# Performance work log

Measured on AMD Instinct MI355X. Metric: run time of the kernel, lower is better.

Reference implementation:

```python
import jax, jax.numpy as jnp
import numpy as np

B, C_IN, C_OUT, N, MODES = 16, 128, 128, 16384, 128

def setup_inputs() -> dict:
    key = jax.random.key(0)
    k1, k2, k3, k4 = jax.random.split(key, 4)
    scale = 1.0 / (C_IN * C_OUT)
    x = jax.random.normal(k1, (B, C_IN, N), dtype=jnp.float32)
    wbases = jax.random.normal(k2, (N, MODES), dtype=jnp.float32)
    bases = jax.random.normal(k3, (N, MODES), dtype=jnp.float32)
    W = scale * jax.random.uniform(k4, (C_IN, C_OUT, MODES), dtype=jnp.float32)
    return {"x": x, "wbases": wbases, "bases": bases, "W": W}

def reference(x, wbases, bases, W):
    # project onto weighted bases: [B, C_in, N] x [N, K] -> [B, C_in, K]
    x_co = jnp.einsum('bcx,xk->bck', x, wbases)
    # per-mode channel mixing: [B, C_in, K] x [C_in, C_out, K] -> [B, C_out, K]
    x_hat = jnp.einsum('bik,iok->bok', x_co, W)
    # reconstruct: [B, C_out, K] x [N, K] -> [B, C_out, N]
    return jnp.einsum('bok,xk->box', x_hat, bases)
```

## Files before the change

kernel.cpp:

```cpp
#include <hip/hip_runtime.h>
#include <hip/hip_bf16.h>
#include <stdint.h>

#define NB 16
#define NC 128
#define NK 128
#define NSP 16384
#define SPLIT 32
#define CHUNK 512

typedef float f32x4 __attribute__((ext_vector_type(4)));
typedef __bf16 bf16x8 __attribute__((ext_vector_type(8)));

__device__ __forceinline__ unsigned short f32_to_bf16(float a) {
  unsigned int u = __float_as_uint(a);
  return (unsigned short)((u + 0x7fffu + ((u >> 16) & 1u)) >> 16);
}

__device__ __forceinline__ unsigned int pack_bf16(float a, float b) {
  unsigned int ua = __float_as_uint(a);
  unsigned int ub = __float_as_uint(b);
  ua = (ua + 0x7fffu + ((ua >> 16) & 1u)) >> 16;
  ub = (ub + 0x7fffu + ((ub >> 16) & 1u)) & 0xffff0000u;
  return ua | ub;
}

__device__ __forceinline__ bf16x8 pack8(float4 a0, float4 a1) {
  uint4 u;
  u.x = pack_bf16(a0.x, a0.y);
  u.y = pack_bf16(a0.z, a0.w);
  u.z = pack_bf16(a1.x, a1.y);
  u.w = pack_bf16(a1.z, a1.w);
  return __builtin_bit_cast(bf16x8, u);
}

__device__ __forceinline__ void gl_lds16(const void* g, void* l) {
  __builtin_amdgcn_global_load_lds(
      (const __attribute__((address_space(1))) unsigned int*)g,
      (__attribute__((address_space(3))) unsigned int*)l, 16, 0, 0);
}

__global__ void k0_prep(const float* __restrict__ wb, unsigned short* __restrict__ wbT,
                        const float* __restrict__ bases, unsigned short* __restrict__ bb) {
  __shared__ float tile[32][33];
  if (blockIdx.x < 2048) {
    int bid = blockIdx.x;
    int kt = (bid & 3) * 32;
    int nt = (bid >> 2) * 32;
    int tx = threadIdx.x & 31;
    int ty = threadIdx.x >> 5;
#pragma unroll
    for (int i = 0; i < 32; i += 8)
      tile[ty + i][tx] = wb[(size_t)(nt + ty + i) * NK + kt + tx];
    __syncthreads();
#pragma unroll
    for (int i = 0; i < 32; i += 8)
      wbT[(size_t)(kt + ty + i) * NSP + nt + tx] = f32_to_bf16(tile[tx][ty + i]);
  } else {
    int i = (blockIdx.x - 2048) * 256 + threadIdx.x;
    float4 v = ((const float4*)bases)[i];
    uint2 o;
    o.x = pack_bf16(v.x, v.y);
    o.y = pack_bf16(v.z, v.w);
    ((uint2*)bb)[i] = o;
  }
}

__global__ __launch_bounds__(256, 4)
void k1_proj(const float* __restrict__ x, const unsigned short* __restrict__ wbT,
             float* __restrict__ part) {
  int blk = blockIdx.x;
  int chunk = blk & 31;
  int bc = blk >> 5;
  int b = bc >> 1;
  int chalf = bc & 1;
  int n0 = chunk * CHUNK;
  __shared__ __align__(16) char lds[2][16384];
  int tid = threadIdx.x;
  int lane = tid & 63;
  int wave = tid >> 6;
  int cbw = (wave & 1) * 32;
  int kbw = (wave >> 1) * 64;
  int r = lane & 15;
  int q = lane >> 4;

  f32x4 acc[2][4];
#pragma unroll
  for (int t = 0; t < 2; ++t)
#pragma unroll
    for (int u = 0; u < 4; ++u) acc[t][u] = (f32x4){0.f, 0.f, 0.f, 0.f};

  const float* aptr = x + (size_t)(b * NC + chalf * 64 + (lane >> 3)) * NSP +
                      n0 + ((lane & 7) ^ (lane >> 3)) * 4;
  const unsigned short* bptr =
      wbT + (size_t)(lane >> 2) * NSP + n0 + (lane & 3) * 8;

#pragma unroll
  for (int j = 0; j < 2; ++j) {
    int i = wave * 2 + j;
    gl_lds16(aptr + (size_t)(8 * i) * NSP, lds[0] + i * 1024);
    gl_lds16(bptr + (size_t)(16 * i) * NSP, lds[0] + 8192 + i * 1024);
  }
  __syncthreads();

#pragma unroll 2
  for (int it = 0; it < CHUNK / 32; ++it) {
    int cur = it & 1;
    if (it + 1 < CHUNK / 32) {
#pragma unroll
      for (int j = 0; j < 2; ++j) {
        int i = wave * 2 + j;
        gl_lds16(aptr + (size_t)(8 * i) * NSP + (it + 1) * 32,
                 lds[cur ^ 1] + i * 1024);
        gl_lds16(bptr + (size_t)(16 * i) * NSP + (it + 1) * 32,
                 lds[cur ^ 1] + 8192 + i * 1024);
      }
    }
    const char* La = lds[cur];
    const char* Lb = lds[cur] + 8192;
    bf16x8 af[2], bf[4];
#pragma unroll
    for (int t = 0; t < 2; ++t) {
      int rw = cbw + 16 * t + r;
      float4 f0 = *(const float4*)(La + rw * 128 + (((2 * q + 0) ^ (r & 7)) << 4));
      float4 f1 = *(const float4*)(La + rw * 128 + (((2 * q + 1) ^ (r & 7)) << 4));
      af[t] = pack8(f0, f1);
    }
#pragma unroll
    for (int u = 0; u < 4; ++u) {
      int rk = kbw + 16 * u + r;
      bf[u] = *(const bf16x8*)(Lb + rk * 64 + q * 16);
    }
#pragma unroll
    for (int t = 0; t < 2; ++t)
#pragma unroll
      for (int u = 0; u < 4; ++u)
        acc[t][u] = __builtin_amdgcn_mfma_f32_16x16x32_bf16(af[t], bf[u],
                                                            acc[t][u], 0, 0, 0);
    __syncthreads();
  }

  float* pp = part + (size_t)(b * SPLIT + chunk) * (NC * NK);
  int rq = q * 4;
#pragma unroll
  for (int t = 0; t < 2; ++t)
#pragma unroll
    for (int u = 0; u < 4; ++u)
#pragma unroll
      for (int v = 0; v < 4; ++v)
        pp[(chalf * 64 + cbw + 16 * t + rq + v) * NK + kbw + 16 * u + r] =
            acc[t][u][v];
}

__global__ __launch_bounds__(256)
void k1b_reduce(const float* __restrict__ part, float* __restrict__ x_co) {
  int idx = blockIdx.x * 256 + threadIdx.x;
  int b = idx >> 13;
  int r2 = idx & 8191;
  const float2* p = (const float2*)(part + (size_t)b * SPLIT * (NC * NK)) + r2;
  float2 s = {0.f, 0.f};
#pragma unroll
  for (int c = 0; c < SPLIT; ++c) {
    float2 v = p[(size_t)c * (NC * NK / 2)];
    s.x += v.x;
    s.y += v.y;
  }
  ((float2*)x_co)[idx] = s;
}

__global__ __launch_bounds__(128)
void k2_mix(const float* __restrict__ x_co, const float* __restrict__ W,
            unsigned short* __restrict__ xhat_bf) {
  int b = blockIdx.x >> 6;
  int o0 = (blockIdx.x & 63) * 2;
  int k = threadIdx.x;
  const float* xc = x_co + (size_t)b * NC * NK + k;
  const float* w0 = W + (size_t)o0 * NK + k;
  float a0 = 0.f, a1 = 0.f;
#pragma unroll 4
  for (int i = 0; i < NC; ++i) {
    float v = xc[(size_t)i * NK];
    a0 += v * w0[(size_t)i * (NC * NK)];
    a1 += v * w0[(size_t)i * (NC * NK) + NK];
  }
  size_t base = ((size_t)b * NC + o0) * NK + k;
  xhat_bf[base] = f32_to_bf16(a0);
  xhat_bf[base + NK] = f32_to_bf16(a1);
}

__global__ __launch_bounds__(256, 4)
void k3_recon(const unsigned short* __restrict__ xhat_bf,
              const unsigned short* __restrict__ bases_bf,
              float* __restrict__ out) {
  int blk = blockIdx.x;
  int mo0 = (blk & 15) * 128;
  int n0 = (blk >> 4) * 256;
  int tid = threadIdx.x;
  int lane = tid & 63;
  int wave = tid >> 6;
  int mb = (wave & 1) * 64;
  int nb = (wave >> 1) * 64;
  int r = lane & 15;
  int q = lane >> 4;
  int rq = q * 4;

  const unsigned short* arow = xhat_bf + (size_t)(mo0 + mb + r) * NK + q * 8;

#pragma unroll
  for (int sub = 0; sub < 2; ++sub) {
    const unsigned short* brow =
        bases_bf + (size_t)(n0 + sub * 128 + nb + r) * NK + q * 8;
    f32x4 acc[4][4];
#pragma unroll
    for (int t = 0; t < 4; ++t)
#pragma unroll
      for (int u = 0; u < 4; ++u) acc[t][u] = (f32x4){0.f, 0.f, 0.f, 0.f};
#pragma unroll
    for (int s = 0; s < 4; ++s) {
      bf16x8 af[4], bf[4];
#pragma unroll
      for (int t = 0; t < 4; ++t)
        af[t] = *(const bf16x8*)(arow + (size_t)t * 16 * NK + s * 32);
#pragma unroll
      for (int u = 0; u < 4; ++u)
        bf[u] = *(const bf16x8*)(brow + (size_t)u * 16 * NK + s * 32);
#pragma unroll
      for (int t = 0; t < 4; ++t)
#pragma unroll
        for (int u = 0; u < 4; ++u)
          acc[t][u] = __builtin_amdgcn_mfma_f32_16x16x32_bf16(af[t], bf[u],
                                                              acc[t][u], 0, 0, 0);
    }
    float* obase = out + (size_t)(mo0 + mb + rq) * NSP + n0 + sub * 128 + nb + r;
#pragma unroll
    for (int t = 0; t < 4; ++t)
#pragma unroll
      for (int u = 0; u < 4; ++u)
#pragma unroll
        for (int v = 0; v < 4; ++v)
          obase[(size_t)(16 * t + v) * NSP + 16 * u] = acc[t][u][v];
  }
}

extern "C" void kernel_launch(void* const* d_in, const int* in_sizes, int n_in,
                              void* d_out, int out_size, void* d_ws, size_t ws_size,
                              hipStream_t stream) {
  const float* x = (const float*)d_in[0];
  const float* wbases = (const float*)d_in[1];
  const float* bases = (const float*)d_in[2];
  const float* W = (const float*)d_in[3];
  float* out = (float*)d_out;

  char* ws = (char*)d_ws;
  if (ws_size < ((size_t)42 << 20)) return;
  unsigned short* wbT = (unsigned short*)(ws);
  unsigned short* bases_bf = (unsigned short*)(ws + ((size_t)4 << 20));
  float* part = (float*)(ws + ((size_t)8 << 20));
  float* x_co = (float*)(ws + ((size_t)40 << 20));
  unsigned short* xhat_bf = (unsigned short*)(ws + ((size_t)41 << 20));

  k0_prep<<<4096, 256, 0, stream>>>(wbases, wbT, bases, bases_bf);
  k1_proj<<<1024, 256, 0, stream>>>(x, wbT, part);
  k1b_reduce<<<512, 256, 0, stream>>>(part, x_co);
  k2_mix<<<NB * NC / 2, 128, 0, stream>>>(x_co, W, xhat_bf);
  k3_recon<<<1024, 256, 0, stream>>>(xhat_bf, bases_bf, out);
}
```

Measured before the change: 324.2 us.

## Triple-buffer projection loads, swap MFMA operands for vector stores, hoist recon A-fragments

The projection kernel moves from a double-buffered to a triple-buffered LDS pipeline. It uses explicit vmcnt waits and a single barrier per iteration, so loads run two stages ahead, at the cost of more LDS per block and lower occupancy (launch bounds drop to 3 waves per EU). Both GEMM kernels swap the MFMA operand order so each lane holds four contiguous output columns, which allows 16-byte vector stores instead of scalar strided stores. The reconstruction kernel loads the xhat fragments once into registers and reuses them across both sub-tiles, which raises register pressure.

```diff
diff --git a/kernel.cpp b/kernel.cpp
--- a/kernel.cpp
+++ b/kernel.cpp
@@ -66,7 +66,7 @@
   }
 }
 
-__global__ __launch_bounds__(256, 4)
+__global__ __launch_bounds__(256, 3)
 void k1_proj(const float* __restrict__ x, const unsigned short* __restrict__ wbT,
              float* __restrict__ part) {
   int blk = blockIdx.x;
@@ -75,7 +75,7 @@
   int b = bc >> 1;
   int chalf = bc & 1;
   int n0 = chunk * CHUNK;
-  __shared__ __align__(16) char lds[2][16384];
+  __shared__ __align__(16) char lds[3][16384];
   int tid = threadIdx.x;
   int lane = tid & 63;
   int wave = tid >> 6;
@@ -95,61 +95,64 @@
   const unsigned short* bptr =
       wbT + (size_t)(lane >> 2) * NSP + n0 + (lane & 3) * 8;
 
-#pragma unroll
-  for (int j = 0; j < 2; ++j) {
-    int i = wave * 2 + j;
-    gl_lds16(aptr + (size_t)(8 * i) * NSP, lds[0] + i * 1024);
-    gl_lds16(bptr + (size_t)(16 * i) * NSP, lds[0] + 8192 + i * 1024);
-  }
-  __syncthreads();
-
-#pragma unroll 2
-  for (int it = 0; it < CHUNK / 32; ++it) {
-    int cur = it & 1;
-    if (it + 1 < CHUNK / 32) {
-#pragma unroll
-      for (int j = 0; j < 2; ++j) {
-        int i = wave * 2 + j;
-        gl_lds16(aptr + (size_t)(8 * i) * NSP + (it + 1) * 32,
-                 lds[cur ^ 1] + i * 1024);
-        gl_lds16(bptr + (size_t)(16 * i) * NSP + (it + 1) * 32,
-                 lds[cur ^ 1] + 8192 + i * 1024);
-      }
-    }
-    const char* La = lds[cur];
-    const char* Lb = lds[cur] + 8192;
-    bf16x8 af[2], bf[4];
-#pragma unroll
-    for (int t = 0; t < 2; ++t) {
-      int rw = cbw + 16 * t + r;
-      float4 f0 = *(const float4*)(La + rw * 128 + (((2 * q + 0) ^ (r & 7)) << 4));
-      float4 f1 = *(const float4*)(La + rw * 128 + (((2 * q + 1) ^ (r & 7)) << 4));
-      af[t] = pack8(f0, f1);
-    }
-#pragma unroll
-    for (int u = 0; u < 4; ++u) {
-      int rk = kbw + 16 * u + r;
-      bf[u] = *(const bf16x8*)(Lb + rk * 64 + q * 16);
-    }
-#pragma unroll
-    for (int t = 0; t < 2; ++t)
-#pragma unroll
-      for (int u = 0; u < 4; ++u)
-        acc[t][u] = __builtin_amdgcn_mfma_f32_16x16x32_bf16(af[t], bf[u],
-                                                            acc[t][u], 0, 0, 0);
-    __syncthreads();
-  }
+#define K1_STAGE(st, buf)                                                     \
+  {                                                                           \
+    _Pragma("unroll") for (int j = 0; j < 2; ++j) {                           \
+      int i = wave * 2 + j;                                                   \
+      gl_lds16(aptr + (size_t)(8 * i) * NSP + (st) * 32, lds[buf] + i * 1024);\
+      gl_lds16(bptr + (size_t)(16 * i) * NSP + (st) * 32,                     \
+               lds[buf] + 8192 + i * 1024);                                   \
+    }                                                                         \
+  }
+
+#define K1_COMPUTE(buf)                                                       \
+  {                                                                           \
+    const char* La = lds[buf];                                                \
+    const char* Lb = lds[buf] + 8192;                                         \
+    bf16x8 af[2], bf[4];                                                      \
+    _Pragma("unroll") for (int t = 0; t < 2; ++t) {                           \
+      int rw = cbw + 16 * t + r;                                              \
+      float4 f0 =                                                             \
+          *(const float4*)(La + rw * 128 + (((2 * q + 0) ^ (r & 7)) << 4));   \
+      float4 f1 =                                                             \
+          *(const float4*)(La + rw * 128 + (((2 * q + 1) ^ (r & 7)) << 4));   \
+      af[t] = pack8(f0, f1);                                                  \
+    }                                                                         \
+    _Pragma("unroll") for (int u = 0; u < 4; ++u) {                           \
+      int rk = kbw + 16 * u + r;                                              \
+      bf[u] = *(const bf16x8*)(Lb + rk * 64 + q * 16);                        \
+    }                                                                         \
+    _Pragma("unroll") for (int t = 0; t < 2; ++t)                             \
+        _Pragma("unroll") for (int u = 0; u < 4; ++u)                         \
+        acc[t][u] = __builtin_amdgcn_mfma_f32_16x16x32_bf16(                  \
+            bf[u], af[t], acc[t][u], 0, 0, 0);                                \
+  }
+
+  K1_STAGE(0, 0);
+  K1_STAGE(1, 1);
+
+#pragma unroll
+  for (int it = 0; it < 15; ++it) {
+    asm volatile("s_waitcnt vmcnt(4)" ::: "memory");
+    __builtin_amdgcn_s_barrier();
+    asm volatile("" ::: "memory");
+    if (it + 2 < 16) K1_STAGE(it + 2, (it + 2) % 3);
+    K1_COMPUTE(it % 3);
+  }
+  asm volatile("s_waitcnt vmcnt(0)" ::: "memory");
+  __builtin_amdgcn_s_barrier();
+  asm volatile("" ::: "memory");
+  K1_COMPUTE(0);
+#undef K1_STAGE
+#undef K1_COMPUTE
 
   float* pp = part + (size_t)(b * SPLIT + chunk) * (NC * NK);
-  int rq = q * 4;
 #pragma unroll
   for (int t = 0; t < 2; ++t)
 #pragma unroll
     for (int u = 0; u < 4; ++u)
-#pragma unroll
-      for (int v = 0; v < 4; ++v)
-        pp[(chalf * 64 + cbw + 16 * t + rq + v) * NK + kbw + 16 * u + r] =
-            acc[t][u][v];
+      *(f32x4*)&pp[(size_t)(chalf * 64 + cbw + 16 * t + r) * NK + kbw + 16 * u +
+                   4 * q] = acc[t][u];
 }
 
 __global__ __launch_bounds__(256)
@@ -202,9 +205,15 @@
   int nb = (wave >> 1) * 64;
   int r = lane & 15;
   int q = lane >> 4;
-  int rq = q * 4;
-
-  const unsigned short* arow = xhat_bf + (size_t)(mo0 + mb + r) * NK + q * 8;
+
+  bf16x8 af[4][4];
+#pragma unroll
+  for (int t = 0; t < 4; ++t)
+#pragma unroll
+    for (int s = 0; s < 4; ++s)
+      af[t][s] = *(const bf16x8*)(xhat_bf +
+                                  (size_t)(mo0 + mb + 16 * t + r) * NK +
+                                  s * 32 + q * 8);
 
 #pragma unroll
   for (int sub = 0; sub < 2; ++sub) {
@@ -217,10 +226,7 @@
       for (int u = 0; u < 4; ++u) acc[t][u] = (f32x4){0.f, 0.f, 0.f, 0.f};
 #pragma unroll
     for (int s = 0; s < 4; ++s) {
-      bf16x8 af[4], bf[4];
-#pragma unroll
-      for (int t = 0; t < 4; ++t)
-        af[t] = *(const bf16x8*)(arow + (size_t)t * 16 * NK + s * 32);
+      bf16x8 bf[4];
 #pragma unroll
       for (int u = 0; u < 4; ++u)
         bf[u] = *(const bf16x8*)(brow + (size_t)u * 16 * NK + s * 32);
@@ -228,17 +234,15 @@
       for (int t = 0; t < 4; ++t)
 #pragma unroll
         for (int u = 0; u < 4; ++u)
-          acc[t][u] = __builtin_amdgcn_mfma_f32_16x16x32_bf16(af[t], bf[u],
-                                                              acc[t][u], 0, 0, 0);
+          acc[t][u] = __builtin_amdgcn_mfma_f32_16x16x32_bf16(
+              bf[u], af[t][s], acc[t][u], 0, 0, 0);
     }
-    float* obase = out + (size_t)(mo0 + mb + rq) * NSP + n0 + sub * 128 + nb + r;
 #pragma unroll
     for (int t = 0; t < 4; ++t)
 #pragma unroll
       for (int u = 0; u < 4; ++u)
-#pragma unroll
-        for (int v = 0; v < 4; ++v)
-          obase[(size_t)(16 * t + v) * NSP + 16 * u] = acc[t][u][v];
+        *(f32x4*)&out[(size_t)(mo0 + mb + 16 * t + r) * NSP + n0 + sub * 128 +
+                      nb + 16 * u + 4 * q] = acc[t][u];
   }
 }
 
```

After: 335.8 us. +3.6%, slower.
